# Kernel optimization log

Measured on AMD Instinct MI355X. Metric: run time of the kernel, lower is better.

The kernel has to match this reference:

```python
import jax, jax.numpy as jnp
from jax import lax
import numpy as np

T, B = 64, 32          # timesteps, n_envs
C_IN, HW = 4, 64
H_LSTM = 256
FEAT = 64 * 4 * 4      # conv output flattened (1024)
FC = 512


def _conv(x, w, b, stride):
    # x: [N,C,H,W], w: [O,I,kh,kw] (torch OIHW), VALID padding like nn.Conv2d default
    y = lax.conv_general_dilated(x, w, (stride, stride), 'VALID',
                                 dimension_numbers=('NCHW', 'OIHW', 'NCHW'))
    return y + b[None, :, None, None]


def setup_inputs() -> dict:
    key = jax.random.key(0)
    ks = jax.random.split(key, 16)
    s = lambda *sh: sh
    d = {
        'x': jax.random.uniform(ks[0], (T * B, C_IN, HW, HW), jnp.float32) * 255.0,
        'done': jax.random.randint(ks[1], (T * B,), 0, 2, jnp.int32),
        'conv1_w': jax.random.normal(ks[2], (32, C_IN, 8, 8), jnp.float32) * 0.05,
        'conv1_b': jnp.zeros((32,), jnp.float32),
        'conv2_w': jax.random.normal(ks[3], (64, 32, 4, 4), jnp.float32) * 0.05,
        'conv2_b': jnp.zeros((64,), jnp.float32),
        'conv3_w': jax.random.normal(ks[4], (64, 64, 3, 3), jnp.float32) * 0.05,
        'conv3_b': jnp.zeros((64,), jnp.float32),
        'fc_w': jax.random.normal(ks[5], (FC, FEAT), jnp.float32) * 0.02,
        'fc_b': jnp.zeros((FC,), jnp.float32),
        'w_ih': jax.random.normal(ks[6], (4 * H_LSTM, FC), jnp.float32) * 0.03,
        'w_hh': jax.random.normal(ks[7], (4 * H_LSTM, H_LSTM), jnp.float32) * 0.03,
        'b_ih': jnp.zeros((4 * H_LSTM,), jnp.float32),
        'b_hh': jnp.zeros((4 * H_LSTM,), jnp.float32),
        'h0': jnp.zeros((1, B, H_LSTM), jnp.float32),
        'c0': jnp.zeros((1, B, H_LSTM), jnp.float32),
    }
    return d


def reference(x, done, conv1_w, conv1_b, conv2_w, conv2_b, conv3_w, conv3_b,
              fc_w, fc_b, w_ih, w_hh, b_ih, b_hh, h0, c0):
    # CNN encoder on x/255
    z = x / 255.0
    z = jax.nn.relu(_conv(z, conv1_w, conv1_b, 4))   # [TB,32,15,15]
    z = jax.nn.relu(_conv(z, conv2_w, conv2_b, 2))   # [TB,64,6,6]
    z = jax.nn.relu(_conv(z, conv3_w, conv3_b, 1))   # [TB,64,4,4]
    z = z.reshape(z.shape[0], -1)                    # [TB,1024]
    feats = jax.nn.relu(z @ fc_w.T + fc_b)           # [TB,512]

    n_envs = h0.shape[1]
    feats = feats.reshape(-1, n_envs, feats.shape[1])        # [T,B,512]
    mask = (1.0 - done.astype(feats.dtype)).reshape(-1, n_envs)  # [T,B]

    H = h0.shape[-1]

    def step(carry, inp):
        h, c = carry                    # [B,H] each
        f_t, m_t = inp                  # [B,512], [B]
        m = m_t[:, None]
        h = h * m
        c = c * m
        gates = f_t @ w_ih.T + b_ih + h @ w_hh.T + b_hh   # [B,4H]
        i, f, g, o = jnp.split(gates, 4, axis=-1)         # torch order: i,f,g,o
        c = jax.nn.sigmoid(f) * c + jax.nn.sigmoid(i) * jnp.tanh(g)
        h = jax.nn.sigmoid(o) * jnp.tanh(c)
        return (h, c), h

    (_, _), hs = lax.scan(step, (h0[0], c0[0]), (feats, mask))  # hs: [T,B,H]
    return hs.reshape(-1, H)   # [T*B, H]
```

## Files before the change

kernel.cpp:

```cpp
#include <hip/hip_runtime.h>
#include <math.h>


#define NIMG 2048

typedef _Float16 half2_t __attribute__((ext_vector_type(2)));
typedef __fp16 fp16x2_t __attribute__((ext_vector_type(2)));

__device__ inline unsigned short f2h_bits(float f) {
    union { _Float16 h; unsigned short u; } x;
    x.h = (_Float16)f;
    return x.u;
}

__device__ inline unsigned pack2_rne(float a, float b) {
    return (unsigned)f2h_bits(a) | ((unsigned)f2h_bits(b) << 16);
}

__device__ inline unsigned pack2_fast(float a, float b) {
#if __has_builtin(__builtin_amdgcn_cvt_pkrtz)
    union { fp16x2_t h; unsigned u; } x;
    x.h = __builtin_amdgcn_cvt_pkrtz(a, b);
    return x.u;
#else
    return pack2_rne(a, b);
#endif
}

__device__ inline float dot2(unsigned hu, unsigned wu, float acc) {
    union { unsigned u; half2_t h; } a, b;
    a.u = hu; b.u = wu;
#if __has_builtin(__builtin_amdgcn_fdot2)
    return __builtin_amdgcn_fdot2(a.h, b.h, acc, false);
#else
    return acc + (float)a.h.x * (float)b.h.x + (float)a.h.y * (float)b.h.y;
#endif
}

__device__ inline float fast_tanh(float x) {
    return 1.0f - 2.0f / (__expf(2.0f * x) + 1.0f);
}

__global__ void transpose_kernel(const float* __restrict__ in, float* __restrict__ out,
                                 int R, int C) {
    int idx = blockIdx.x * 256 + threadIdx.x;
    if (idx < R * C) {
        int r = idx / C, c = idx - r * C;
        out[c * R + r] = in[idx];
    }
}

__global__ void pack_pairs_kernel(const float* __restrict__ src,
                                  unsigned* __restrict__ dst, int total) {
    int idx = blockIdx.x * 256 + threadIdx.x;
    if (idx < total) {
        const float* s = src + (size_t)idx * 2;
        dst[idx] = pack2_rne(s[0], s[1]);
    }
}

__global__ void pack_whh_pairs_kernel(const float* __restrict__ whh,
                                      unsigned* __restrict__ wp) {
    int idx = blockIdx.x * 256 + threadIdx.x;
    if (idx >= 131072) return;
    int d4 = idx >> 12;
    int rem = idx & 4095;
    int row = rem >> 2;
    int j = idx & 3;
    int k0 = d4 * 8 + j * 2;
    const float* src = whh + (size_t)row * 256 + k0;
    wp[idx] = pack2_rne(src[0], src[1]);
}

__global__ void pack_w1_kernel(const float* __restrict__ w1, unsigned* __restrict__ w1p) {
    int idx = blockIdx.x * 256 + threadIdx.x;
    if (idx >= 4096) return;
    int oc = idx >> 7, rem = idx & 127;
    int ic = rem >> 5, ky = (rem >> 2) & 7, kxp = rem & 3;
    const float* src = w1 + (((size_t)oc * 4 + ic) * 8 + ky) * 8 + kxp * 2;
    w1p[idx] = pack2_rne(src[0], src[1]);
}

__global__ void pack_w2_kernel(const float* __restrict__ w2, unsigned* __restrict__ w2p) {
    int idx = blockIdx.x * 256 + threadIdx.x;
    if (idx >= 16384) return;
    int p = idx >> 6, oc = idx & 63;
    int ic = p >> 3, ky = (p >> 1) & 3, kxp = p & 1;
    const float* src = w2 + (size_t)oc * 512 + ic * 16 + ky * 4 + kxp * 2;
    w2p[idx] = pack2_rne(src[0], src[1]);
}

__global__ __launch_bounds__(1024) void conv1_kernel(const float* __restrict__ x,
                                                     const unsigned* __restrict__ w1p,
                                                     const float* __restrict__ b,
                                                     unsigned short* __restrict__ z1) {
    __shared__ unsigned short xs[4 * 64 * 64];
    int n = blockIdx.x;
    int tid = threadIdx.x;
    const float* xp = x + (size_t)n * 16384;
    const float inv = 1.0f / 255.0f;
    for (int i = tid * 4; i < 16384; i += 4096) {
        float4 v = *(const float4*)(xp + i);
        uint2 q;
        q.x = pack2_fast(v.x * inv, v.y * inv);
        q.y = pack2_fast(v.z * inv, v.w * inv);
        *(uint2*)&xs[i] = q;
    }
    __syncthreads();
    int lane = tid & 63, wave = tid >> 6;
    int gg = __builtin_amdgcn_readfirstlane(wave & 3);
    int pos = (wave >> 2) * 64 + lane;
    if (pos < 225) {
        int oy = pos / 15, ox = pos - oy * 15;
        float acc[8];
        const float* bp = b + gg * 8;
#pragma unroll
        for (int u = 0; u < 8; ++u) acc[u] = bp[u];
        for (int ic = 0; ic < 4; ++ic) {
#pragma unroll
            for (int ky = 0; ky < 8; ++ky) {
                const unsigned short* row = &xs[(ic * 64 + oy * 4 + ky) * 64 + ox * 4];
                uint2 qa = *(const uint2*)row;
                uint2 qb = *(const uint2*)(row + 4);
                const unsigned* wp = w1p + ((((gg * 8) * 4 + ic) * 8 + ky) * 4);
#pragma unroll
                for (int u = 0; u < 8; ++u) {
                    const unsigned* wu = wp + u * 128;
                    acc[u] = dot2(qa.x, wu[0], acc[u]);
                    acc[u] = dot2(qa.y, wu[1], acc[u]);
                    acc[u] = dot2(qb.x, wu[2], acc[u]);
                    acc[u] = dot2(qb.y, wu[3], acc[u]);
                }
            }
        }
        unsigned short* op = z1 + (size_t)n * 7680 + (gg * 8) * 240 + oy * 16 + ox;
#pragma unroll
        for (int u = 0; u < 8; ++u) op[u * 240] = f2h_bits(fmaxf(acc[u], 0.0f));
    }
}

__global__ __launch_bounds__(768) void conv2_kernel(const unsigned short* __restrict__ z1,
                                                    const unsigned* __restrict__ w2p,
                                                    const float* __restrict__ bias,
                                                    float* __restrict__ out) {
    __shared__ unsigned short xs[2][32 * 15 * 16];
    int tid = threadIdx.x;
    int n0 = blockIdx.x * 2;
#pragma unroll
    for (int img = 0; img < 2; ++img) {
        const unsigned* src = (const unsigned*)(z1 + (size_t)(n0 + img) * 7680);
        unsigned* dst = (unsigned*)xs[img];
        for (int i = tid; i < 3840; i += 768) dst[i] = src[i];
    }
    __syncthreads();
    int lane = tid & 63, wave = tid >> 6;
    int img = wave / 6;
    int oy = wave - img * 6;
    int n = n0 + img;
    float bv = bias[lane];
    float* op = out + (size_t)n * 2304 + lane * 36;
    float acc[6];
#pragma unroll
    for (int u = 0; u < 6; ++u) acc[u] = bv;
    for (int ic = 0; ic < 32; ++ic) {
#pragma unroll
        for (int ky = 0; ky < 4; ++ky) {
            const unsigned short* row = &xs[img][(ic * 15 + oy * 2 + ky) * 16];
            uint4 pa = *(const uint4*)row;
            uint4 pb = *(const uint4*)(row + 8);
            unsigned p[8] = {pa.x, pa.y, pa.z, pa.w, pb.x, pb.y, pb.z, pb.w};
            const unsigned* wpp = w2p + ((ic * 4 + ky) * 2) * 64 + lane;
            unsigned wa = wpp[0];
            unsigned wb = wpp[64];
#pragma unroll
            for (int u = 0; u < 6; ++u) {
                acc[u] = dot2(p[u], wa, acc[u]);
                acc[u] = dot2(p[u + 1], wb, acc[u]);
            }
        }
    }
#pragma unroll
    for (int u = 0; u < 6; ++u) op[oy * 6 + u] = fmaxf(acc[u], 0.0f);
}

__global__ __launch_bounds__(512) void conv3_kernel(const float* __restrict__ x,
                                                    const float* __restrict__ wt,
                                                    const float* __restrict__ bias,
                                                    unsigned* __restrict__ outp) {
    __shared__ float xs[4][64 * 6 * 8];
    int tid = threadIdx.x;
    int n0 = blockIdx.x * 4;
    for (int img = 0; img < 4; ++img) {
        const float* src = x + (size_t)(n0 + img) * 2304;
        for (int s = tid; s < 2304; s += 512) {
            int ic = s / 36;
            int rem = s - ic * 36;
            int r = rem / 6;
            int c = rem - r * 6;
            xs[img][(ic * 6 + r) * 8 + c] = src[s];
        }
    }
    __syncthreads();
    int lane = tid & 63, wave = tid >> 6;
    int img = wave >> 1;
    int half = wave & 1;
    int n = n0 + img;
    float bv = bias[lane];
    unsigned* op = outp + (size_t)n * 512 + lane * 8;
    for (int q = 0; q < 2; ++q) {
        int oy = half * 2 + q;
        float acc[4];
#pragma unroll
        for (int u = 0; u < 4; ++u) acc[u] = bv;
        for (int ic = 0; ic < 64; ++ic) {
#pragma unroll
            for (int ky = 0; ky < 3; ++ky) {
                const float* xrow = &xs[img][(ic * 6 + oy + ky) * 8];
                float xr[8];
                *(float4*)&xr[0] = *(const float4*)&xrow[0];
                *(float4*)&xr[4] = *(const float4*)&xrow[4];
                const float* wp = wt + ((ic * 3 + ky) * 3) * 64 + lane;
#pragma unroll
                for (int kx = 0; kx < 3; ++kx) {
                    float wv = wp[kx * 64];
#pragma unroll
                    for (int u = 0; u < 4; ++u) acc[u] += xr[u + kx] * wv;
                }
            }
        }
        float a0 = fmaxf(acc[0], 0.0f), a1 = fmaxf(acc[1], 0.0f);
        float a2 = fmaxf(acc[2], 0.0f), a3 = fmaxf(acc[3], 0.0f);
        op[oy * 2 + 0] = pack2_rne(a0, a1);
        op[oy * 2 + 1] = pack2_rne(a2, a3);
    }
}

__global__ __launch_bounds__(256) void gemm_bt_h(const unsigned* __restrict__ A,
                                                 const unsigned* __restrict__ B,
                                                 const float* __restrict__ bias,
                                                 const float* __restrict__ bias2,
                                                 float* __restrict__ C,
                                                 unsigned* __restrict__ Ch,
                                                 int M, int N, int Kp, int relu) {
    __shared__ unsigned As[16][66];
    __shared__ unsigned Bs[16][66];
    int tid = threadIdx.x;
    int m0 = blockIdx.y * 64, n0 = blockIdx.x * 64;
    int tx = tid & 15, ty = tid >> 4;
    int lr = tid >> 2;
    int lk = (tid & 3) * 4;
    const unsigned* Ap = A + (size_t)(m0 + lr) * Kp + lk;
    const unsigned* Bp = B + (size_t)(n0 + lr) * Kp + lk;
    float acc[4][4];
#pragma unroll
    for (int i = 0; i < 4; ++i)
#pragma unroll
        for (int j = 0; j < 4; ++j) acc[i][j] = 0.0f;

    uint4 av = *(const uint4*)Ap;
    uint4 bv = *(const uint4*)Bp;
    for (int k0 = 0; k0 < Kp; k0 += 16) {
        __syncthreads();
        As[lk + 0][lr] = av.x;
        As[lk + 1][lr] = av.y;
        As[lk + 2][lr] = av.z;
        As[lk + 3][lr] = av.w;
        Bs[lk + 0][lr] = bv.x;
        Bs[lk + 1][lr] = bv.y;
        Bs[lk + 2][lr] = bv.z;
        Bs[lk + 3][lr] = bv.w;
        __syncthreads();
        if (k0 + 16 < Kp) {
            av = *(const uint4*)(Ap + k0 + 16);
            bv = *(const uint4*)(Bp + k0 + 16);
        }
#pragma unroll
        for (int kk = 0; kk < 16; ++kk) {
            unsigned a[4], b[4];
            *(uint4*)a = *(const uint4*)&As[kk][ty * 4];
            *(uint4*)b = *(const uint4*)&Bs[kk][tx * 4];
#pragma unroll
            for (int i = 0; i < 4; ++i)
#pragma unroll
                for (int j = 0; j < 4; ++j) acc[i][j] = dot2(a[i], b[j], acc[i][j]);
        }
    }
    float bb[4];
#pragma unroll
    for (int j = 0; j < 4; ++j) {
        float v = bias[n0 + tx * 4 + j];
        if (bias2) v += bias2[n0 + tx * 4 + j];
        bb[j] = v;
    }
#pragma unroll
    for (int i = 0; i < 4; ++i) {
        float4 o;
        o.x = acc[i][0] + bb[0];
        o.y = acc[i][1] + bb[1];
        o.z = acc[i][2] + bb[2];
        o.w = acc[i][3] + bb[3];
        if (relu) {
            o.x = fmaxf(o.x, 0.0f);
            o.y = fmaxf(o.y, 0.0f);
            o.z = fmaxf(o.z, 0.0f);
            o.w = fmaxf(o.w, 0.0f);
        }
        size_t mrow = (size_t)(m0 + ty * 4 + i);
        if (C) *(float4*)&C[mrow * N + n0 + tx * 4] = o;
        if (Ch) {
            unsigned* cp = Ch + mrow * (N >> 1) + (n0 >> 1) + tx * 2;
            cp[0] = pack2_rne(o.x, o.y);
            cp[1] = pack2_rne(o.z, o.w);
        }
    }
}

__global__ __launch_bounds__(1024) void lstm_kernel(const float* __restrict__ gi,
                                                    const unsigned* __restrict__ wp,
                                                    const int* __restrict__ done,
                                                    const float* __restrict__ h0,
                                                    const float* __restrict__ c0,
                                                    float* __restrict__ out) {
    __shared__ alignas(16) unsigned wo[32768];
    __shared__ alignas(16) unsigned h2u[128];
    __shared__ float xch[4096];
    int b = blockIdx.x, tt = threadIdx.x;
    int u = tt & 255, q = tt >> 8;
    int q8 = q * 8;

    const uint4* wsrc = (const uint4*)wp;

    {
        uint4* dst = (uint4*)wo;
        for (int i4 = tt; i4 < 8192; i4 += 1024) {
            int d4 = i4 >> 8, r = i4 & 255;
            dst[i4] = wsrc[d4 * 1024 + 768 + r];
        }
    }

#define LDW(j)                                              \
    uint4 wi##j = wsrc[(q8 + j) * 1024 + u];                \
    uint4 wf##j = wsrc[(q8 + j) * 1024 + 256 + u];          \
    uint4 wg##j = wsrc[(q8 + j) * 1024 + 512 + u];
    LDW(0) LDW(1) LDW(2) LDW(3) LDW(4) LDW(5) LDW(6) LDW(7)
#undef LDW

    if (tt < 128) {
        h2u[tt] = pack2_rne(h0[b * 256 + 2 * tt], h0[b * 256 + 2 * tt + 1]);
    }
    float c = 0.0f;
    float gv0 = 0.f, gv1 = 0.f, gv2 = 0.f, gv3 = 0.f;
    int dn = done[b];
    const float* gbase = gi + (size_t)b * 1024;
    if (q == 0) {
        c = c0[b * 256 + u];
        gv0 = gbase[u];
        gv1 = gbase[256 + u];
        gv2 = gbase[512 + u];
        gv3 = gbase[768 + u];
    }
    __syncthreads();

    const uint4* h2u4 = (const uint4*)h2u;
    const uint4* wo4 = (const uint4*)wo;

    for (int step = 0; step < 64; ++step) {
        int dnn = 0;
        if (step < 63) dnn = done[(step + 1) * 32 + b];
        float nx0 = 0.f, nx1 = 0.f, nx2 = 0.f, nx3 = 0.f;
        if (q == 0 && step < 63) {
            const float* gb = gbase + (size_t)(step + 1) * 32768;
            nx0 = gb[u];
            nx1 = gb[256 + u];
            nx2 = gb[512 + u];
            nx3 = gb[768 + u];
        }

        float pI = 0.f, pF = 0.f, pG = 0.f, pO = 0.f;
        if (!dn) {
#define MV(j) {                                                         \
        uint4 ha = h2u4[q8 + j];          \
        uint4 wv = wo4[(q8 + j) * 256 + u];   \
        pI = dot2(ha.x, wi##j.x, pI); pI = dot2(ha.y, wi##j.y, pI);     \
        pI = dot2(ha.z, wi##j.z, pI); pI = dot2(ha.w, wi##j.w, pI);     \
        pF = dot2(ha.x, wf##j.x, pF); pF = dot2(ha.y, wf##j.y, pF);     \
        pF = dot2(ha.z, wf##j.z, pF); pF = dot2(ha.w, wf##j.w, pF);     \
        pG = dot2(ha.x, wg##j.x, pG); pG = dot2(ha.y, wg##j.y, pG);     \
        pG = dot2(ha.z, wg##j.z, pG); pG = dot2(ha.w, wg##j.w, pG);     \
        pO = dot2(ha.x, wv.x, pO);    pO = dot2(ha.y, wv.y, pO);        \
        pO = dot2(ha.z, wv.z, pO);    pO = dot2(ha.w, wv.w, pO); }
            MV(0) MV(1) MV(2) MV(3) MV(4) MV(5) MV(6) MV(7)
#undef MV
        }

        xch[q * 1024 + u] = pI;
        xch[q * 1024 + 256 + u] = pF;
        xch[q * 1024 + 512 + u] = pG;
        xch[q * 1024 + 768 + u] = pO;
        __syncthreads();

        if (q == 0) {
            float m = 1.0f - (float)dn;
            float sI = xch[u] + xch[1024 + u] + xch[2048 + u] + xch[3072 + u];
            float sF = xch[256 + u] + xch[1280 + u] + xch[2304 + u] + xch[3328 + u];
            float sG = xch[512 + u] + xch[1536 + u] + xch[2560 + u] + xch[3584 + u];
            float sO = xch[768 + u] + xch[1792 + u] + xch[2816 + u] + xch[3840 + u];
            float g_i = gv0 + m * sI;
            float g_f = gv1 + m * sF;
            float g_g = gv2 + m * sG;
            float g_o = gv3 + m * sO;
            float si = 1.0f / (1.0f + __expf(-g_i));
            float sf = 1.0f / (1.0f + __expf(-g_f));
            float so = 1.0f / (1.0f + __expf(-g_o));
            float tg = fast_tanh(g_g);
            c = sf * (c * m) + si * tg;
            float hn = so * fast_tanh(c);
            out[((size_t)step * 32 + b) * 256 + u] = hn;
            float hn2 = __shfl_xor(hn, 1);
            if ((u & 1) == 0) {
                unsigned lo = f2h_bits(hn);
                unsigned hi = f2h_bits(hn2);
                h2u[u >> 1] = lo | (hi << 16);
            }
        }
        __syncthreads();

        gv0 = nx0; gv1 = nx1; gv2 = nx2; gv3 = nx3;
        dn = dnn;
    }
}

extern "C" void kernel_launch(void* const* d_in, const int* in_sizes, int n_in,
                              void* d_out, int out_size, void* d_ws, size_t ws_size,
                              hipStream_t stream) {
    const float* x    = (const float*)d_in[0];
    const int*   done = (const int*)d_in[1];
    const float* w1   = (const float*)d_in[2];
    const float* b1   = (const float*)d_in[3];
    const float* w2   = (const float*)d_in[4];
    const float* b2   = (const float*)d_in[5];
    const float* w3   = (const float*)d_in[6];
    const float* b3   = (const float*)d_in[7];
    const float* fcw  = (const float*)d_in[8];
    const float* fcb  = (const float*)d_in[9];
    const float* wih  = (const float*)d_in[10];
    const float* whh  = (const float*)d_in[11];
    const float* bih  = (const float*)d_in[12];
    const float* bhh  = (const float*)d_in[13];
    const float* h0   = (const float*)d_in[14];
    const float* c0   = (const float*)d_in[15];
    float* out = (float*)d_out;
    float* ws = (float*)d_ws;

    unsigned short* z1u = (unsigned short*)(ws + 0);
    float* z2     = ws + 8000000;
    unsigned* z3h = (unsigned*)(ws + 0);
    unsigned* featsh = (unsigned*)(ws + 2097152);
    float* gi     = ws + 3145728;
    unsigned* fcwph = (unsigned*)(ws + 8000000);
    unsigned* wihph = (unsigned*)(ws + 8300000);
    float* w3t    = ws + 13000000;
    unsigned* w1p = (unsigned*)(ws + 13100000);
    unsigned* w2p = (unsigned*)(ws + 13200000);
    unsigned* wp  = (unsigned*)(ws + 13300000);

    transpose_kernel<<<(64 * 576 + 255) / 256, 256, 0, stream>>>(w3, w3t, 64, 576);
    pack_whh_pairs_kernel<<<512, 256, 0, stream>>>(whh, wp);
    pack_w1_kernel<<<16, 256, 0, stream>>>(w1, w1p);
    pack_w2_kernel<<<64, 256, 0, stream>>>(w2, w2p);

    conv1_kernel<<<NIMG, 1024, 0, stream>>>(x, w1p, b1, z1u);
    conv2_kernel<<<NIMG / 2, 768, 0, stream>>>(z1u, w2p, b2, z2);
    conv3_kernel<<<NIMG / 4, 512, 0, stream>>>(z2, w3t, b3, z3h);

    pack_pairs_kernel<<<(512 * 512 + 255) / 256, 256, 0, stream>>>(fcw, fcwph, 512 * 512);
    pack_pairs_kernel<<<(1024 * 256 + 255) / 256, 256, 0, stream>>>(wih, wihph, 1024 * 256);

    gemm_bt_h<<<dim3(512 / 64, NIMG / 64), 256, 0, stream>>>(
        z3h, fcwph, fcb, nullptr, nullptr, featsh, NIMG, 512, 512, 1);
    gemm_bt_h<<<dim3(1024 / 64, NIMG / 64), 256, 0, stream>>>(
        featsh, wihph, bih, bhh, gi, nullptr, NIMG, 1024, 256, 0);

    lstm_kernel<<<32, 1024, 0, stream>>>(gi, wp, done, h0, c0, out);
}
```

Before: 566.0 us.

## Convert conv3 to fp16 dot2 with LDS-staged weights and merge weight packing

conv2 now writes its output as packed fp16 channel pairs instead of fp32. conv3 is rewritten to use packed fp16 dot2 with its weights staged in shared memory, and each wave computes a full 4x4 output for one image, 8 images per block. All six weight-packing kernels are merged into one launch. The aim is to cut conv2/conv3 memory traffic, conv3 FMA count and launch overhead, at the cost of extra fp16 rounding on the conv2 activations and a large LDS footprint per conv3 block.

```diff
diff --git a/kernel.cpp b/kernel.cpp
--- a/kernel.cpp
+++ b/kernel.cpp
@@ -41,53 +41,61 @@
     return 1.0f - 2.0f / (__expf(2.0f * x) + 1.0f);
 }
 
-__global__ void transpose_kernel(const float* __restrict__ in, float* __restrict__ out,
-                                 int R, int C) {
+__global__ void pack_all_kernel(const float* __restrict__ whh,
+                                const float* __restrict__ w1,
+                                const float* __restrict__ w2,
+                                const float* __restrict__ w3,
+                                const float* __restrict__ fcw,
+                                const float* __restrict__ wih,
+                                unsigned* __restrict__ wp,
+                                unsigned* __restrict__ w1p,
+                                unsigned* __restrict__ w2p,
+                                unsigned* __restrict__ w3ph,
+                                unsigned* __restrict__ fcwph,
+                                unsigned* __restrict__ wihph) {
     int idx = blockIdx.x * 256 + threadIdx.x;
-    if (idx < R * C) {
-        int r = idx / C, c = idx - r * C;
-        out[c * R + r] = in[idx];
-    }
-}
-
-__global__ void pack_pairs_kernel(const float* __restrict__ src,
-                                  unsigned* __restrict__ dst, int total) {
-    int idx = blockIdx.x * 256 + threadIdx.x;
-    if (idx < total) {
-        const float* s = src + (size_t)idx * 2;
-        dst[idx] = pack2_rne(s[0], s[1]);
-    }
-}
-
-__global__ void pack_whh_pairs_kernel(const float* __restrict__ whh,
-                                      unsigned* __restrict__ wp) {
-    int idx = blockIdx.x * 256 + threadIdx.x;
-    if (idx >= 131072) return;
-    int d4 = idx >> 12;
-    int rem = idx & 4095;
-    int row = rem >> 2;
-    int j = idx & 3;
-    int k0 = d4 * 8 + j * 2;
-    const float* src = whh + (size_t)row * 256 + k0;
-    wp[idx] = pack2_rne(src[0], src[1]);
-}
-
-__global__ void pack_w1_kernel(const float* __restrict__ w1, unsigned* __restrict__ w1p) {
-    int idx = blockIdx.x * 256 + threadIdx.x;
-    if (idx >= 4096) return;
-    int oc = idx >> 7, rem = idx & 127;
-    int ic = rem >> 5, ky = (rem >> 2) & 7, kxp = rem & 3;
-    const float* src = w1 + (((size_t)oc * 4 + ic) * 8 + ky) * 8 + kxp * 2;
-    w1p[idx] = pack2_rne(src[0], src[1]);
-}
-
-__global__ void pack_w2_kernel(const float* __restrict__ w2, unsigned* __restrict__ w2p) {
-    int idx = blockIdx.x * 256 + threadIdx.x;
-    if (idx >= 16384) return;
-    int p = idx >> 6, oc = idx & 63;
-    int ic = p >> 3, ky = (p >> 1) & 3, kxp = p & 1;
-    const float* src = w2 + (size_t)oc * 512 + ic * 16 + ky * 4 + kxp * 2;
-    w2p[idx] = pack2_rne(src[0], src[1]);
+    if (idx < 131072) {
+        int d4 = idx >> 12, rem = idx & 4095, row = rem >> 2, j = idx & 3;
+        const float* s = whh + (size_t)row * 256 + d4 * 8 + j * 2;
+        wp[idx] = pack2_rne(s[0], s[1]);
+        return;
+    }
+    idx -= 131072;
+    if (idx < 4096) {
+        int oc = idx >> 7, rem = idx & 127;
+        int ic = rem >> 5, ky = (rem >> 2) & 7, kxp = rem & 3;
+        const float* s = w1 + (((size_t)oc * 4 + ic) * 8 + ky) * 8 + kxp * 2;
+        w1p[idx] = pack2_rne(s[0], s[1]);
+        return;
+    }
+    idx -= 4096;
+    if (idx < 16384) {
+        int p = idx >> 6, oc = idx & 63;
+        int ic = p >> 3, ky = (p >> 1) & 3, kxp = p & 1;
+        const float* s = w2 + (size_t)oc * 512 + ic * 16 + ky * 4 + kxp * 2;
+        w2p[idx] = pack2_rne(s[0], s[1]);
+        return;
+    }
+    idx -= 16384;
+    if (idx < 18432) {
+        int oc = idx & 63, rest = idx >> 6;
+        int icp = rest & 31, kxy = rest >> 5;
+        int ky = kxy / 3, kx = kxy - ky * 3;
+        const float* s = w3 + (((size_t)oc * 64 + icp * 2) * 3 + ky) * 3 + kx;
+        w3ph[idx] = pack2_rne(s[0], s[9]);
+        return;
+    }
+    idx -= 18432;
+    if (idx < 262144) {
+        const float* s = fcw + (size_t)idx * 2;
+        fcwph[idx] = pack2_rne(s[0], s[1]);
+        return;
+    }
+    idx -= 262144;
+    if (idx < 262144) {
+        const float* s = wih + (size_t)idx * 2;
+        wihph[idx] = pack2_rne(s[0], s[1]);
+    }
 }
 
 __global__ __launch_bounds__(1024) void conv1_kernel(const float* __restrict__ x,
@@ -122,10 +130,10 @@
                 const unsigned short* row = &xs[(ic * 64 + oy * 4 + ky) * 64 + ox * 4];
                 uint2 qa = *(const uint2*)row;
                 uint2 qb = *(const uint2*)(row + 4);
-                const unsigned* wp = w1p + ((((gg * 8) * 4 + ic) * 8 + ky) * 4);
+                const unsigned* wpt = w1p + ((((gg * 8) * 4 + ic) * 8 + ky) * 4);
 #pragma unroll
                 for (int u = 0; u < 8; ++u) {
-                    const unsigned* wu = wp + u * 128;
+                    const unsigned* wu = wpt + u * 128;
                     acc[u] = dot2(qa.x, wu[0], acc[u]);
                     acc[u] = dot2(qa.y, wu[1], acc[u]);
                     acc[u] = dot2(qb.x, wu[2], acc[u]);
@@ -142,7 +150,7 @@
 __global__ __launch_bounds__(768) void conv2_kernel(const unsigned short* __restrict__ z1,
                                                     const unsigned* __restrict__ w2p,
                                                     const float* __restrict__ bias,
-                                                    float* __restrict__ out) {
+                                                    unsigned* __restrict__ z2h) {
     __shared__ unsigned short xs[2][32 * 15 * 16];
     int tid = threadIdx.x;
     int n0 = blockIdx.x * 2;
@@ -158,7 +166,6 @@
     int oy = wave - img * 6;
     int n = n0 + img;
     float bv = bias[lane];
-    float* op = out + (size_t)n * 2304 + lane * 36;
     float acc[6];
 #pragma unroll
     for (int u = 0; u < 6; ++u) acc[u] = bv;
@@ -179,57 +186,65 @@
             }
         }
     }
-#pragma unroll
-    for (int u = 0; u < 6; ++u) op[oy * 6 + u] = fmaxf(acc[u], 0.0f);
-}
-
-__global__ __launch_bounds__(512) void conv3_kernel(const float* __restrict__ x,
-                                                    const float* __restrict__ wt,
+    unsigned* zb = z2h + (size_t)n * 1152;
+#pragma unroll
+    for (int u = 0; u < 6; ++u) {
+        float a = fmaxf(acc[u], 0.0f);
+        float a2 = __shfl_xor(a, 1);
+        if ((lane & 1) == 0) {
+            zb[(oy * 6 + u) * 32 + (lane >> 1)] = pack2_rne(a, a2);
+        }
+    }
+}
+
+__global__ __launch_bounds__(512) void conv3_kernel(const unsigned* __restrict__ z2h,
+                                                    const unsigned* __restrict__ w3ph,
                                                     const float* __restrict__ bias,
                                                     unsigned* __restrict__ outp) {
-    __shared__ float xs[4][64 * 6 * 8];
+    __shared__ unsigned w3s[18432];
+    __shared__ unsigned xs8[8][1152];
     int tid = threadIdx.x;
-    int n0 = blockIdx.x * 4;
-    for (int img = 0; img < 4; ++img) {
-        const float* src = x + (size_t)(n0 + img) * 2304;
-        for (int s = tid; s < 2304; s += 512) {
-            int ic = s / 36;
-            int rem = s - ic * 36;
-            int r = rem / 6;
-            int c = rem - r * 6;
-            xs[img][(ic * 6 + r) * 8 + c] = src[s];
-        }
+    int n0 = blockIdx.x * 8;
+    for (int i = tid; i < 18432; i += 512) w3s[i] = w3ph[i];
+    for (int i = tid; i < 8 * 1152; i += 512) {
+        int img = i / 1152;
+        int rem = i - img * 1152;
+        int pos = rem >> 5, icp = rem & 31;
+        xs8[img][icp * 36 + pos] = z2h[(size_t)(n0 + img) * 1152 + rem];
     }
     __syncthreads();
-    int lane = tid & 63, wave = tid >> 6;
-    int img = wave >> 1;
-    int half = wave & 1;
+    int lane = tid & 63, img = tid >> 6;
     int n = n0 + img;
     float bv = bias[lane];
+    float acc[4][4];
+#pragma unroll
+    for (int oy = 0; oy < 4; ++oy)
+#pragma unroll
+        for (int ox = 0; ox < 4; ++ox) acc[oy][ox] = bv;
+    const unsigned* wb = w3s + lane;
+    const unsigned* xb = xs8[img];
+    for (int icp = 0; icp < 32; ++icp) {
+        unsigned xr[36];
+#pragma unroll
+        for (int p4 = 0; p4 < 9; ++p4)
+            *(uint4*)&xr[p4 * 4] = *(const uint4*)&xb[icp * 36 + p4 * 4];
+#pragma unroll
+        for (int ky = 0; ky < 3; ++ky)
+#pragma unroll
+            for (int kx = 0; kx < 3; ++kx) {
+                unsigned w = wb[((ky * 3 + kx) * 32 + icp) * 64];
+#pragma unroll
+                for (int oy = 0; oy < 4; ++oy)
+#pragma unroll
+                    for (int ox = 0; ox < 4; ++ox)
+                        acc[oy][ox] = dot2(xr[(oy + ky) * 6 + ox + kx], w, acc[oy][ox]);
+            }
+    }
     unsigned* op = outp + (size_t)n * 512 + lane * 8;
-    for (int q = 0; q < 2; ++q) {
-        int oy = half * 2 + q;
-        float acc[4];
-#pragma unroll
-        for (int u = 0; u < 4; ++u) acc[u] = bv;
-        for (int ic = 0; ic < 64; ++ic) {
-#pragma unroll
-            for (int ky = 0; ky < 3; ++ky) {
-                const float* xrow = &xs[img][(ic * 6 + oy + ky) * 8];
-                float xr[8];
-                *(float4*)&xr[0] = *(const float4*)&xrow[0];
-                *(float4*)&xr[4] = *(const float4*)&xrow[4];
-                const float* wp = wt + ((ic * 3 + ky) * 3) * 64 + lane;
-#pragma unroll
-                for (int kx = 0; kx < 3; ++kx) {
-                    float wv = wp[kx * 64];
-#pragma unroll
-                    for (int u = 0; u < 4; ++u) acc[u] += xr[u + kx] * wv;
-                }
-            }
-        }
-        float a0 = fmaxf(acc[0], 0.0f), a1 = fmaxf(acc[1], 0.0f);
-        float a2 = fmaxf(acc[2], 0.0f), a3 = fmaxf(acc[3], 0.0f);
+#pragma unroll
+    for (int oy = 0; oy < 4; ++oy) {
+        float a0 = fmaxf(acc[oy][0], 0.f), a1 = fmaxf(acc[oy][1], 0.f);
+        float a2 = fmaxf(acc[oy][2], 0.f), a3 = fmaxf(acc[oy][3], 0.f);
         op[oy * 2 + 0] = pack2_rne(a0, a1);
         op[oy * 2 + 1] = pack2_rne(a2, a3);
     }
@@ -453,28 +468,23 @@
     float* ws = (float*)d_ws;
 
     unsigned short* z1u = (unsigned short*)(ws + 0);
-    float* z2     = ws + 8000000;
+    unsigned* z2h = (unsigned*)(ws + 8000000);
     unsigned* z3h = (unsigned*)(ws + 0);
     unsigned* featsh = (unsigned*)(ws + 2097152);
     float* gi     = ws + 3145728;
-    unsigned* fcwph = (unsigned*)(ws + 8000000);
-    unsigned* wihph = (unsigned*)(ws + 8300000);
-    float* w3t    = ws + 13000000;
+    unsigned* fcwph = (unsigned*)(ws + 10400000);
+    unsigned* wihph = (unsigned*)(ws + 10700000);
+    unsigned* w3ph  = (unsigned*)(ws + 13000000);
     unsigned* w1p = (unsigned*)(ws + 13100000);
     unsigned* w2p = (unsigned*)(ws + 13200000);
     unsigned* wp  = (unsigned*)(ws + 13300000);
 
-    transpose_kernel<<<(64 * 576 + 255) / 256, 256, 0, stream>>>(w3, w3t, 64, 576);
-    pack_whh_pairs_kernel<<<512, 256, 0, stream>>>(whh, wp);
-    pack_w1_kernel<<<16, 256, 0, stream>>>(w1, w1p);
-    pack_w2_kernel<<<64, 256, 0, stream>>>(w2, w2p);
+    pack_all_kernel<<<(694272 + 255) / 256, 256, 0, stream>>>(
+        whh, w1, w2, w3, fcw, wih, wp, w1p, w2p, w3ph, fcwph, wihph);
 
     conv1_kernel<<<NIMG, 1024, 0, stream>>>(x, w1p, b1, z1u);
-    conv2_kernel<<<NIMG / 2, 768, 0, stream>>>(z1u, w2p, b2, z2);
-    conv3_kernel<<<NIMG / 4, 512, 0, stream>>>(z2, w3t, b3, z3h);
-
-    pack_pairs_kernel<<<(512 * 512 + 255) / 256, 256, 0, stream>>>(fcw, fcwph, 512 * 512);
-    pack_pairs_kernel<<<(1024 * 256 + 255) / 256, 256, 0, stream>>>(wih, wihph, 1024 * 256);
+    conv2_kernel<<<NIMG / 2, 768, 0, stream>>>(z1u, w2p, b2, z2h);
+    conv3_kernel<<<NIMG / 8, 512, 0, stream>>>(z2h, w3ph, b3, z3h);
 
     gemm_bt_h<<<dim3(512 / 64, NIMG / 64), 256, 0, stream>>>(
         z3h, fcwph, fcb, nullptr, nullptr, featsh, NIMG, 512, 512, 1);
```

After: 520.3 us. 1.09x faster.
